# Kernel optimization log

Hardware: AMD Instinct MI355X
Metric: run time of the kernel (lower is better)

## Reference

```python
import jax, jax.numpy as jnp
import numpy as np

EMBED_DIM = 1024
NUM_HEADS = 16
HEAD_DIM = EMBED_DIM // NUM_HEADS


def setup_inputs() -> dict:
    key = jax.random.key(0)
    k1, k2, k3, k4, k5 = jax.random.split(key, 5)
    B, T, C = 4, 2048, EMBED_DIM
    scale = 1.0 / np.sqrt(C)
    return {
        "x": jax.random.normal(k1, (B, T, C), dtype=jnp.float32),
        "W_qkv": jax.random.normal(k2, (3 * C, C), dtype=jnp.float32) * scale,
        "b_qkv": jax.random.normal(k3, (3 * C,), dtype=jnp.float32) * 0.02,
        "W_proj": jax.random.normal(k4, (C, C), dtype=jnp.float32) * scale,
        "b_proj": jax.random.normal(k5, (C,), dtype=jnp.float32) * 0.02,
    }


def reference(x, W_qkv, b_qkv, W_proj, b_proj):
    B, T, C = x.shape
    H, D = NUM_HEADS, HEAD_DIM
    qkv = x @ W_qkv.T + b_qkv                      # [B,T,3C]
    q, k, v = jnp.split(qkv, 3, axis=-1)
    q = q.reshape(B, T, H, D).transpose(0, 2, 1, 3)  # [B,H,T,D]
    k = k.reshape(B, T, H, D).transpose(0, 2, 1, 3)
    v = v.reshape(B, T, H, D).transpose(0, 2, 1, 3)
    scores = jnp.einsum("bhqd,bhkd->bhqk", q, k) / np.sqrt(D)  # [B,H,T,T]
    causal = jnp.tril(jnp.ones((T, T), dtype=bool))
    scores = jnp.where(causal, scores, -jnp.inf)
    attn = jax.nn.softmax(scores, axis=-1)
    out = jnp.einsum("bhqk,bhkd->bhqd", attn, v)   # [B,H,T,D]
    out = out.transpose(0, 2, 1, 3).reshape(B, T, C)
    return out @ W_proj.T + b_proj
```

## Files before the change

kernel.cpp:

```cpp
#include <hip/hip_runtime.h>
#include <math.h>

#define EMBED 1024
#define NHEAD 16
#define HDIM  64
#define SEQT  2048
#define BATCH 4

typedef __bf16 bf16x4 __attribute__((ext_vector_type(4)));
typedef __bf16 bf16x8 __attribute__((ext_vector_type(8)));
typedef float  f32x4  __attribute__((ext_vector_type(4)));

#define AS1 __attribute__((address_space(1)))
#define AS3 __attribute__((address_space(3)))
#define GLD_LDS16(gp, lp) __builtin_amdgcn_global_load_lds( \
    (const AS1 unsigned int*)(gp), (AS3 unsigned int*)(lp), 16, 0, 0)

#define QSCALE 0.180336880f

__device__ __forceinline__ unsigned short f2bf_hw(float f) {
    union { __bf16 h; unsigned short u; } c; c.h = (__bf16)f; return c.u;
}

__global__ __launch_bounds__(256)
void cvt_all(const float* __restrict__ x, const float* __restrict__ wq,
             const float* __restrict__ wp,
             unsigned short* __restrict__ xb, unsigned short* __restrict__ wqb,
             unsigned short* __restrict__ wpb)
{
    const int N1 = 2097152;
    const int N2 = 786432;
    int i = blockIdx.x * 256 + threadIdx.x;
    const float4* src; ushort4* dst; int j;
    if (i < N1)            { src = (const float4*)x;  dst = (ushort4*)xb;  j = i; }
    else if (i < N1 + N2)  { src = (const float4*)wq; dst = (ushort4*)wqb; j = i - N1; }
    else                   { src = (const float4*)wp; dst = (ushort4*)wpb; j = i - N1 - N2; }
    float4 v = src[j];
    ushort4 o;
    o.x = f2bf_hw(v.x); o.y = f2bf_hw(v.y); o.z = f2bf_hw(v.z); o.w = f2bf_hw(v.w);
    dst[j] = o;
}

template<int MODE>
__global__ __launch_bounds__(256)
void gemm_bt_mfma(const unsigned short* __restrict__ A, const unsigned short* __restrict__ Bw,
                  const float* __restrict__ bias,
                  void* out0, void* out1, void* out2,
                  int M, int N, int K)
{
    __shared__ __align__(16) unsigned short Asm[2][128 * 64];
    __shared__ __align__(16) unsigned short Bsm[2][128 * 64];

    const int tid  = threadIdx.x;
    const int lane = tid & 63;
    const int wave = tid >> 6;
    const int wm = wave >> 1, wn = wave & 1;
    const int col = lane & 15, quad = lane >> 4;
    const long m0 = (long)blockIdx.y * 128, n0 = (long)blockIdx.x * 128;

    f32x4 acc[4][4];
#pragma unroll
    for (int mi = 0; mi < 4; mi++)
#pragma unroll
        for (int ni = 0; ni < 4; ni++) acc[mi][ni] = (f32x4){0.f, 0.f, 0.f, 0.f};

    const int srow  = tid >> 3;
    const int gslot = (tid & 7) ^ (srow & 7);
    const unsigned short* Ag = A  + (m0 + srow) * K + gslot * 8;
    const unsigned short* Bg = Bw + (n0 + srow) * K + gslot * 8;

#define STAGE(buf_, kk_) do { \
    _Pragma("unroll") for (int r_ = 0; r_ < 4; r_++) { \
        GLD_LDS16(Ag + (long)(r_ * 32) * K + (kk_), &Asm[buf_][0] + r_ * 2048 + tid * 8); \
        GLD_LDS16(Bg + (long)(r_ * 32) * K + (kk_), &Bsm[buf_][0] + r_ * 2048 + tid * 8); \
    } } while (0)

    const int cs0 = ((quad    ) ^ (col & 7)) * 8;
    const int cs1 = ((quad + 4) ^ (col & 7)) * 8;

    STAGE(0, 0);

    const int iters = K >> 6;
    for (int it = 0; it < iters; it++) {
        const int cur = it & 1;
        __builtin_amdgcn_s_waitcnt(0x0F70);
        __syncthreads();
        if (it + 1 < iters)
            STAGE(cur ^ 1, (it + 1) * 64);

        bf16x8 af[4][2], bf[4][2];
#pragma unroll
        for (int mi = 0; mi < 4; mi++) {
            const int row = wm * 64 + mi * 16 + col;
            af[mi][0] = *(const bf16x8*)&Asm[cur][row * 64 + cs0];
            af[mi][1] = *(const bf16x8*)&Asm[cur][row * 64 + cs1];
        }
#pragma unroll
        for (int ni = 0; ni < 4; ni++) {
            const int row = wn * 64 + ni * 16 + col;
            bf[ni][0] = *(const bf16x8*)&Bsm[cur][row * 64 + cs0];
            bf[ni][1] = *(const bf16x8*)&Bsm[cur][row * 64 + cs1];
        }
#pragma unroll
        for (int mi = 0; mi < 4; mi++)
#pragma unroll
            for (int ni = 0; ni < 4; ni++) {
                acc[mi][ni] = __builtin_amdgcn_mfma_f32_16x16x32_bf16(af[mi][0], bf[ni][0], acc[mi][ni], 0, 0, 0);
                acc[mi][ni] = __builtin_amdgcn_mfma_f32_16x16x32_bf16(af[mi][1], bf[ni][1], acc[mi][ni], 0, 0, 0);
            }
    }
#undef STAGE

#pragma unroll
    for (int mi = 0; mi < 4; mi++) {
#pragma unroll
        for (int ni = 0; ni < 4; ni++) {
            long n = n0 + wn * 64 + ni * 16 + col;
            float bv = bias[n];
#pragma unroll
            for (int r = 0; r < 4; r++) {
                long m = m0 + wm * 64 + mi * 16 + quad * 4 + r;
                float v = acc[mi][ni][r] + bv;
                if (MODE == 0) {
                    ((float*)out0)[m * N + n] = v;
                } else {
                    int which = (int)(n >> 10);
                    int c = (int)(n & 1023);
                    int h = c >> 6, d = c & 63;
                    int b = (int)(m >> 11), t = (int)(m & 2047);
                    long bh = (long)(b * NHEAD + h);
                    if (which == 0)      ((unsigned short*)out0)[(bh * SEQT + t) * HDIM + d] = f2bf_hw(v * QSCALE);
                    else if (which == 1) ((unsigned short*)out1)[(bh * SEQT + t) * HDIM + d] = f2bf_hw(v);
                    else                 ((unsigned short*)out2)[(bh * HDIM + d) * SEQT + t] = f2bf_hw(v);
                }
            }
        }
    }
}

#define PPAD 72

__global__ __launch_bounds__(256, 3)
void flash_attn_mfma4(const unsigned short* __restrict__ Qb,
                      const unsigned short* __restrict__ Kb,
                      const unsigned short* __restrict__ Vt,
                      unsigned short* __restrict__ Ob)
{
    __shared__ __align__(16) unsigned short P_lds[128 * PPAD];
    __shared__ __align__(16) unsigned short K_lds[2][64 * 64];
    __shared__ __align__(16) unsigned short V_lds[2][64 * 64];
    __shared__ __align__(16) float L_lds[128];

    const int tid  = threadIdx.x;
    const int lane = tid & 63;
    const int wave = tid >> 6;
    const int col  = lane & 15;
    const int quad = lane >> 4;

    const int idx = blockIdx.x;
    const int qt = 15 - (idx >> 6);
    const int hb = idx & 63;
    const int h = hb & 15, b = hb >> 4;
    const int q0 = qt * 128;
    const long bh = (long)(b * NHEAD + h);
    const unsigned short* Kbh = Kb + bh * SEQT * HDIM;
    const unsigned short* Vbh = Vt + bh * HDIM * SEQT;
    const int ktiles = 2 * qt + 2;

    const int r0 = tid >> 3,         c0 = (tid & 7) ^ (r0 & 7);
    const int r1 = (tid + 256) >> 3, c1 = (tid & 7) ^ (r1 & 7);

    bf16x8 qf[2][2];
#pragma unroll
    for (int ni = 0; ni < 2; ni++) {
        const unsigned short* qrow = Qb + (bh * SEQT + q0 + wave * 32 + ni * 16 + col) * HDIM;
        qf[ni][0] = *(const bf16x8*)(qrow + quad * 8);
        qf[ni][1] = *(const bf16x8*)(qrow + 32 + quad * 8);
    }

    GLD_LDS16(Kbh + r0 * HDIM + c0 * 8,        &K_lds[0][0] + tid * 8);
    GLD_LDS16(Kbh + r1 * HDIM + c1 * 8,        &K_lds[0][0] + 2048 + tid * 8);
    GLD_LDS16(Vbh + (long)r0 * SEQT + c0 * 8,  &V_lds[0][0] + tid * 8);
    GLD_LDS16(Vbh + (long)r1 * SEQT + c1 * 8,  &V_lds[0][0] + 2048 + tid * 8);

    f32x4 o[2][4];
#pragma unroll
    for (int mi = 0; mi < 2; mi++)
#pragma unroll
        for (int dt = 0; dt < 4; dt++) o[mi][dt] = (f32x4){0.f, 0.f, 0.f, 0.f};
    float rs[2] = {0.f, 0.f};

    const int cswz0 = quad ^ (col & 7);
    const int cswz1 = (quad + 4) ^ (col & 7);

    for (int kt = 0; kt < ktiles; kt++) {
        const int cur = kt & 1;
        __builtin_amdgcn_s_waitcnt(0x0F70);
        __syncthreads();
        if (kt + 1 < ktiles) {
            const int k0n = (kt + 1) * 64, nxt = cur ^ 1;
            GLD_LDS16(Kbh + (k0n + r0) * HDIM + c0 * 8,       &K_lds[nxt][0] + tid * 8);
            GLD_LDS16(Kbh + (k0n + r1) * HDIM + c1 * 8,       &K_lds[nxt][0] + 2048 + tid * 8);
            GLD_LDS16(Vbh + (long)r0 * SEQT + k0n + c0 * 8,   &V_lds[nxt][0] + tid * 8);
            GLD_LDS16(Vbh + (long)r1 * SEQT + k0n + c1 * 8,   &V_lds[nxt][0] + 2048 + tid * 8);
        }

        const unsigned short* Kc = &K_lds[cur][0];
        f32x4 st[4][2];
        __builtin_amdgcn_s_setprio(1);
#pragma unroll
        for (int mt = 0; mt < 4; mt++) {
            const int row = mt * 16 + col;
            bf16x8 kf0 = *(const bf16x8*)&Kc[row * 64 + cswz0 * 8];
            bf16x8 kf1 = *(const bf16x8*)&Kc[row * 64 + cswz1 * 8];
#pragma unroll
            for (int ni = 0; ni < 2; ni++) {
                f32x4 acc = (f32x4){0.f, 0.f, 0.f, 0.f};
                acc = __builtin_amdgcn_mfma_f32_16x16x32_bf16(kf0, qf[ni][0], acc, 0, 0, 0);
                acc = __builtin_amdgcn_mfma_f32_16x16x32_bf16(kf1, qf[ni][1], acc, 0, 0, 0);
                st[mt][ni] = acc;
            }
        }
        __builtin_amdgcn_s_setprio(0);
        const int k0 = kt * 64;
        if (kt >= 2 * qt) {
#pragma unroll
            for (int mt = 0; mt < 4; mt++) {
                const int keybase = k0 + mt * 16 + quad * 4;
#pragma unroll
                for (int ni = 0; ni < 2; ni++) {
                    const int qg = q0 + wave * 32 + ni * 16 + col;
#pragma unroll
                    for (int r = 0; r < 4; r++)
                        if (keybase + r > qg) st[mt][ni][r] = -INFINITY;
                }
            }
        }

#pragma unroll
        for (int mt = 0; mt < 4; mt++)
#pragma unroll
            for (int ni = 0; ni < 2; ni++) {
                f32x4 p;
#pragma unroll
                for (int r = 0; r < 4; r++) p[r] = __builtin_amdgcn_exp2f(st[mt][ni][r]);
                rs[ni] += (p[0] + p[1]) + (p[2] + p[3]);
                bf16x4 pb = __builtin_convertvector(p, bf16x4);
                *(bf16x4*)&P_lds[(wave * 32 + ni * 16 + col) * PPAD + mt * 16 + quad * 4] = pb;
            }

        const unsigned short* Vc = &V_lds[cur][0];
        __builtin_amdgcn_s_setprio(1);
#pragma unroll
        for (int mi = 0; mi < 2; mi++) {
            const unsigned short* prow = &P_lds[(wave * 32 + mi * 16 + col) * PPAD];
            bf16x8 pf0 = *(const bf16x8*)(prow + quad * 8);
            bf16x8 pf1 = *(const bf16x8*)(prow + 32 + quad * 8);
#pragma unroll
            for (int dt = 0; dt < 4; dt++) {
                const int row = dt * 16 + col;
                bf16x8 vf0 = *(const bf16x8*)&Vc[row * 64 + cswz0 * 8];
                bf16x8 vf1 = *(const bf16x8*)&Vc[row * 64 + cswz1 * 8];
                o[mi][dt] = __builtin_amdgcn_mfma_f32_16x16x32_bf16(pf0, vf0, o[mi][dt], 0, 0, 0);
                o[mi][dt] = __builtin_amdgcn_mfma_f32_16x16x32_bf16(pf1, vf1, o[mi][dt], 0, 0, 0);
            }
        }
        __builtin_amdgcn_s_setprio(0);
    }

#pragma unroll
    for (int ni = 0; ni < 2; ni++) {
        rs[ni] += __shfl_xor(rs[ni], 16);
        rs[ni] += __shfl_xor(rs[ni], 32);
        if (quad == 0) L_lds[wave * 32 + ni * 16 + col] = rs[ni];
    }
    __syncthreads();
    f32x4 lf[2];
#pragma unroll
    for (int mi = 0; mi < 2; mi++)
        lf[mi] = *(const f32x4*)&L_lds[wave * 32 + mi * 16 + quad * 4];

#pragma unroll
    for (int mi = 0; mi < 2; mi++)
#pragma unroll
        for (int r = 0; r < 4; r++) {
            float inv = 1.f / lf[mi][r];
            int t = q0 + wave * 32 + mi * 16 + quad * 4 + r;
            unsigned short* orow = Ob + ((long)(b * SEQT + t)) * EMBED + h * HDIM;
#pragma unroll
            for (int dt = 0; dt < 4; dt++)
                orow[dt * 16 + col] = f2bf_hw(o[mi][dt][r] * inv);
        }
}

extern "C" void kernel_launch(void* const* d_in, const int* in_sizes, int n_in,
                              void* d_out, int out_size, void* d_ws, size_t ws_size,
                              hipStream_t stream)
{
    const float* x     = (const float*)d_in[0];
    const float* Wqkv  = (const float*)d_in[1];
    const float* bqkv  = (const float*)d_in[2];
    const float* Wproj = (const float*)d_in[3];
    const float* bproj = (const float*)d_in[4];
    float* out = (float*)d_out;

    const long Mbt = (long)BATCH * SEQT;
    const long per = (long)BATCH * NHEAD * SEQT * HDIM;

    unsigned short* xb  = (unsigned short*)d_ws;
    unsigned short* wqb = xb  + per;
    unsigned short* wpb = wqb + 3 * EMBED * EMBED;
    unsigned short* Qb  = wpb + EMBED * EMBED;
    unsigned short* Kb  = Qb + per;
    unsigned short* Vt  = Kb + per;
    unsigned short* Ob  = Vt + per;

    cvt_all<<<12288, 256, 0, stream>>>(x, Wqkv, Wproj, xb, wqb, wpb);

    dim3 g1(3 * EMBED / 128, Mbt / 128);
    gemm_bt_mfma<1><<<g1, 256, 0, stream>>>(xb, wqb, bqkv, Qb, Kb, Vt,
                                            (int)Mbt, 3 * EMBED, EMBED);

    flash_attn_mfma4<<<1024, 256, 0, stream>>>(Qb, Kb, Vt, Ob);

    dim3 g3(EMBED / 128, Mbt / 128);
    gemm_bt_mfma<0><<<g3, 256, 0, stream>>>(Ob, wpb, bproj, out, nullptr, nullptr,
                                            (int)Mbt, EMBED, EMBED);
}
```

Before: 250.7 us.

## Register-prefetch single-buffered K/V tiles and interleave causal block order

New measurement: 395.8 us. 1.58x slower.

```diff
diff --git a/kernel.cpp b/kernel.cpp
--- a/kernel.cpp
+++ b/kernel.cpp
@@ -10,6 +10,7 @@
 typedef __bf16 bf16x4 __attribute__((ext_vector_type(4)));
 typedef __bf16 bf16x8 __attribute__((ext_vector_type(8)));
 typedef float  f32x4  __attribute__((ext_vector_type(4)));
+typedef unsigned short u16x8 __attribute__((ext_vector_type(8)));
 
 #define AS1 __attribute__((address_space(1)))
 #define AS3 __attribute__((address_space(3)))
@@ -140,15 +141,15 @@
 
 #define PPAD 72
 
-__global__ __launch_bounds__(256, 3)
-void flash_attn_mfma4(const unsigned short* __restrict__ Qb,
+__global__ __launch_bounds__(256, 4)
+void flash_attn_mfma5(const unsigned short* __restrict__ Qb,
                       const unsigned short* __restrict__ Kb,
                       const unsigned short* __restrict__ Vt,
                       unsigned short* __restrict__ Ob)
 {
     __shared__ __align__(16) unsigned short P_lds[128 * PPAD];
-    __shared__ __align__(16) unsigned short K_lds[2][64 * 64];
-    __shared__ __align__(16) unsigned short V_lds[2][64 * 64];
+    __shared__ __align__(16) unsigned short K_lds[64 * 64];
+    __shared__ __align__(16) unsigned short V_lds[64 * 64];
     __shared__ __align__(16) float L_lds[128];
 
     const int tid  = threadIdx.x;
@@ -158,7 +159,8 @@
     const int quad = lane >> 4;
 
     const int idx = blockIdx.x;
-    const int qt = 15 - (idx >> 6);
+    const int g = idx >> 6;
+    const int qt = (g & 1) ? (g >> 1) : (15 - (g >> 1));
     const int hb = idx & 63;
     const int h = hb & 15, b = hb >> 4;
     const int q0 = qt * 128;
@@ -167,8 +169,17 @@
     const unsigned short* Vbh = Vt + bh * HDIM * SEQT;
     const int ktiles = 2 * qt + 2;
 
-    const int r0 = tid >> 3,         c0 = (tid & 7) ^ (r0 & 7);
-    const int r1 = (tid + 256) >> 3, c1 = (tid & 7) ^ (r1 & 7);
+    const int r0   = tid >> 3;
+    const int slot = tid & 7;
+    const int ws   = (slot ^ (r0 & 7)) * 8;
+    unsigned short* kw0 = &K_lds[r0 * 64 + ws];
+    unsigned short* kw1 = &K_lds[(r0 + 32) * 64 + ws];
+    unsigned short* vw0 = &V_lds[r0 * 64 + ws];
+    unsigned short* vw1 = &V_lds[(r0 + 32) * 64 + ws];
+    const unsigned short* Kg0 = Kbh + r0 * HDIM + slot * 8;
+    const unsigned short* Kg1 = Kbh + (r0 + 32) * HDIM + slot * 8;
+    const unsigned short* Vg0 = Vbh + (long)r0 * SEQT + slot * 8;
+    const unsigned short* Vg1 = Vbh + (long)(r0 + 32) * SEQT + slot * 8;
 
     bf16x8 qf[2][2];
 #pragma unroll
@@ -178,10 +189,15 @@
         qf[ni][1] = *(const bf16x8*)(qrow + 32 + quad * 8);
     }
 
-    GLD_LDS16(Kbh + r0 * HDIM + c0 * 8,        &K_lds[0][0] + tid * 8);
-    GLD_LDS16(Kbh + r1 * HDIM + c1 * 8,        &K_lds[0][0] + 2048 + tid * 8);
-    GLD_LDS16(Vbh + (long)r0 * SEQT + c0 * 8,  &V_lds[0][0] + tid * 8);
-    GLD_LDS16(Vbh + (long)r1 * SEQT + c1 * 8,  &V_lds[0][0] + 2048 + tid * 8);
+    {
+        u16x8 kr0 = *(const u16x8*)Kg0;
+        u16x8 kr1 = *(const u16x8*)Kg1;
+        u16x8 vr0 = *(const u16x8*)Vg0;
+        u16x8 vr1 = *(const u16x8*)Vg1;
+        *(u16x8*)kw0 = kr0; *(u16x8*)kw1 = kr1;
+        *(u16x8*)vw0 = vr0; *(u16x8*)vw1 = vr1;
+    }
+    __syncthreads();
 
     f32x4 o[2][4];
 #pragma unroll
@@ -193,26 +209,24 @@
     const int cswz0 = quad ^ (col & 7);
     const int cswz1 = (quad + 4) ^ (col & 7);
 
+    u16x8 kr0, kr1, vr0, vr1;
     for (int kt = 0; kt < ktiles; kt++) {
-        const int cur = kt & 1;
-        __builtin_amdgcn_s_waitcnt(0x0F70);
-        __syncthreads();
         if (kt + 1 < ktiles) {
-            const int k0n = (kt + 1) * 64, nxt = cur ^ 1;
-            GLD_LDS16(Kbh + (k0n + r0) * HDIM + c0 * 8,       &K_lds[nxt][0] + tid * 8);
-            GLD_LDS16(Kbh + (k0n + r1) * HDIM + c1 * 8,       &K_lds[nxt][0] + 2048 + tid * 8);
-            GLD_LDS16(Vbh + (long)r0 * SEQT + k0n + c0 * 8,   &V_lds[nxt][0] + tid * 8);
-            GLD_LDS16(Vbh + (long)r1 * SEQT + k0n + c1 * 8,   &V_lds[nxt][0] + 2048 + tid * 8);
-        }
-
-        const unsigned short* Kc = &K_lds[cur][0];
+            const int t1 = (kt + 1) * 64;
+            kr0 = *(const u16x8*)(Kg0 + (long)t1 * HDIM);
+            kr1 = *(const u16x8*)(Kg1 + (long)t1 * HDIM);
+            vr0 = *(const u16x8*)(Vg0 + t1);
+            vr1 = *(const u16x8*)(Vg1 + t1);
+        }
+        __builtin_amdgcn_sched_barrier(0);
+
         f32x4 st[4][2];
         __builtin_amdgcn_s_setprio(1);
 #pragma unroll
         for (int mt = 0; mt < 4; mt++) {
             const int row = mt * 16 + col;
-            bf16x8 kf0 = *(const bf16x8*)&Kc[row * 64 + cswz0 * 8];
-            bf16x8 kf1 = *(const bf16x8*)&Kc[row * 64 + cswz1 * 8];
+            bf16x8 kf0 = *(const bf16x8*)&K_lds[row * 64 + cswz0 * 8];
+            bf16x8 kf1 = *(const bf16x8*)&K_lds[row * 64 + cswz1 * 8];
 #pragma unroll
             for (int ni = 0; ni < 2; ni++) {
                 f32x4 acc = (f32x4){0.f, 0.f, 0.f, 0.f};
@@ -249,7 +263,6 @@
                 *(bf16x4*)&P_lds[(wave * 32 + ni * 16 + col) * PPAD + mt * 16 + quad * 4] = pb;
             }
 
-        const unsigned short* Vc = &V_lds[cur][0];
         __builtin_amdgcn_s_setprio(1);
 #pragma unroll
         for (int mi = 0; mi < 2; mi++) {
@@ -259,13 +272,20 @@
 #pragma unroll
             for (int dt = 0; dt < 4; dt++) {
                 const int row = dt * 16 + col;
-                bf16x8 vf0 = *(const bf16x8*)&Vc[row * 64 + cswz0 * 8];
-                bf16x8 vf1 = *(const bf16x8*)&Vc[row * 64 + cswz1 * 8];
+                bf16x8 vf0 = *(const bf16x8*)&V_lds[row * 64 + cswz0 * 8];
+                bf16x8 vf1 = *(const bf16x8*)&V_lds[row * 64 + cswz1 * 8];
                 o[mi][dt] = __builtin_amdgcn_mfma_f32_16x16x32_bf16(pf0, vf0, o[mi][dt], 0, 0, 0);
                 o[mi][dt] = __builtin_amdgcn_mfma_f32_16x16x32_bf16(pf1, vf1, o[mi][dt], 0, 0, 0);
             }
         }
         __builtin_amdgcn_s_setprio(0);
+
+        __syncthreads();
+        if (kt + 1 < ktiles) {
+            *(u16x8*)kw0 = kr0; *(u16x8*)kw1 = kr1;
+            *(u16x8*)vw0 = vr0; *(u16x8*)vw1 = vr1;
+        }
+        __syncthreads();
     }
 
 #pragma unroll
@@ -321,7 +341,7 @@
     gemm_bt_mfma<1><<<g1, 256, 0, stream>>>(xb, wqb, bqkv, Qb, Kb, Vt,
                                             (int)Mbt, 3 * EMBED, EMBED);
 
-    flash_attn_mfma4<<<1024, 256, 0, stream>>>(Qb, Kb, Vt, Ob);
+    flash_attn_mfma5<<<1024, 256, 0, stream>>>(Qb, Kb, Vt, Ob);
 
     dim3 g3(EMBED / 128, Mbt / 128);
     gemm_bt_mfma<0><<<g3, 256, 0, stream>>>(Ob, wpb, bproj, out, nullptr, nullptr,
```

## Switch flash attention to 32x32x16 MFMA and keep P in registers

Applied to the files above, without the earlier changes.

After: 256.9 us. 1.02x slower.

```diff
diff --git a/kernel.cpp b/kernel.cpp
--- a/kernel.cpp
+++ b/kernel.cpp
@@ -10,6 +10,7 @@
 typedef __bf16 bf16x4 __attribute__((ext_vector_type(4)));
 typedef __bf16 bf16x8 __attribute__((ext_vector_type(8)));
 typedef float  f32x4  __attribute__((ext_vector_type(4)));
+typedef float  f32x16 __attribute__((ext_vector_type(16)));
 
 #define AS1 __attribute__((address_space(1)))
 #define AS3 __attribute__((address_space(3)))
@@ -20,6 +21,9 @@
 
 __device__ __forceinline__ unsigned short f2bf_hw(float f) {
     union { __bf16 h; unsigned short u; } c; c.h = (__bf16)f; return c.u;
+}
+__device__ __forceinline__ unsigned pk2(float a, float b) {
+    union { __bf16 h[2]; unsigned u; } c; c.h[0] = (__bf16)a; c.h[1] = (__bf16)b; return c.u;
 }
 
 __global__ __launch_bounds__(256)
@@ -138,24 +142,21 @@
     }
 }
 
-#define PPAD 72
-
 __global__ __launch_bounds__(256, 3)
-void flash_attn_mfma4(const unsigned short* __restrict__ Qb,
+void flash_attn_mfma6(const unsigned short* __restrict__ Qb,
                       const unsigned short* __restrict__ Kb,
                       const unsigned short* __restrict__ Vt,
                       unsigned short* __restrict__ Ob)
 {
-    __shared__ __align__(16) unsigned short P_lds[128 * PPAD];
     __shared__ __align__(16) unsigned short K_lds[2][64 * 64];
     __shared__ __align__(16) unsigned short V_lds[2][64 * 64];
-    __shared__ __align__(16) float L_lds[128];
 
     const int tid  = threadIdx.x;
     const int lane = tid & 63;
     const int wave = tid >> 6;
-    const int col  = lane & 15;
-    const int quad = lane >> 4;
+    const int lq   = lane & 31;
+    const int hi   = lane >> 5;
+    const int l7   = lane & 7;
 
     const int idx = blockIdx.x;
     const int qt = 15 - (idx >> 6);
@@ -166,32 +167,26 @@
     const unsigned short* Kbh = Kb + bh * SEQT * HDIM;
     const unsigned short* Vbh = Vt + bh * HDIM * SEQT;
     const int ktiles = 2 * qt + 2;
-
-    const int r0 = tid >> 3,         c0 = (tid & 7) ^ (r0 & 7);
-    const int r1 = (tid + 256) >> 3, c1 = (tid & 7) ^ (r1 & 7);
-
-    bf16x8 qf[2][2];
-#pragma unroll
-    for (int ni = 0; ni < 2; ni++) {
-        const unsigned short* qrow = Qb + (bh * SEQT + q0 + wave * 32 + ni * 16 + col) * HDIM;
-        qf[ni][0] = *(const bf16x8*)(qrow + quad * 8);
-        qf[ni][1] = *(const bf16x8*)(qrow + 32 + quad * 8);
-    }
-
-    GLD_LDS16(Kbh + r0 * HDIM + c0 * 8,        &K_lds[0][0] + tid * 8);
-    GLD_LDS16(Kbh + r1 * HDIM + c1 * 8,        &K_lds[0][0] + 2048 + tid * 8);
-    GLD_LDS16(Vbh + (long)r0 * SEQT + c0 * 8,  &V_lds[0][0] + tid * 8);
-    GLD_LDS16(Vbh + (long)r1 * SEQT + c1 * 8,  &V_lds[0][0] + 2048 + tid * 8);
-
-    f32x4 o[2][4];
-#pragma unroll
-    for (int mi = 0; mi < 2; mi++)
-#pragma unroll
-        for (int dt = 0; dt < 4; dt++) o[mi][dt] = (f32x4){0.f, 0.f, 0.f, 0.f};
-    float rs[2] = {0.f, 0.f};
-
-    const int cswz0 = quad ^ (col & 7);
-    const int cswz1 = (quad + 4) ^ (col & 7);
+    const int qg = q0 + wave * 32 + lq;
+
+    const int r0 = tid >> 3;
+    const int cs = (tid & 7) ^ (r0 & 7);
+
+    bf16x8 qf[4];
+    {
+        const unsigned short* qrow = Qb + (bh * SEQT + qg) * HDIM;
+#pragma unroll
+        for (int c = 0; c < 4; c++)
+            qf[c] = *(const bf16x8*)(qrow + c * 16 + hi * 8);
+    }
+
+    GLD_LDS16(Kbh + r0 * HDIM + cs * 8,              &K_lds[0][0] + tid * 8);
+    GLD_LDS16(Kbh + (r0 + 32) * HDIM + cs * 8,       &K_lds[0][0] + 2048 + tid * 8);
+    GLD_LDS16(Vbh + (long)r0 * SEQT + cs * 8,        &V_lds[0][0] + tid * 8);
+    GLD_LDS16(Vbh + (long)(r0 + 32) * SEQT + cs * 8, &V_lds[0][0] + 2048 + tid * 8);
+
+    f32x16 ot0 = {}, ot1 = {};
+    float rs = 0.f;
 
     for (int kt = 0; kt < ktiles; kt++) {
         const int cur = kt & 1;
@@ -199,98 +194,92 @@
         __syncthreads();
         if (kt + 1 < ktiles) {
             const int k0n = (kt + 1) * 64, nxt = cur ^ 1;
-            GLD_LDS16(Kbh + (k0n + r0) * HDIM + c0 * 8,       &K_lds[nxt][0] + tid * 8);
-            GLD_LDS16(Kbh + (k0n + r1) * HDIM + c1 * 8,       &K_lds[nxt][0] + 2048 + tid * 8);
-            GLD_LDS16(Vbh + (long)r0 * SEQT + k0n + c0 * 8,   &V_lds[nxt][0] + tid * 8);
-            GLD_LDS16(Vbh + (long)r1 * SEQT + k0n + c1 * 8,   &V_lds[nxt][0] + 2048 + tid * 8);
+            GLD_LDS16(Kbh + (k0n + r0) * HDIM + cs * 8,            &K_lds[nxt][0] + tid * 8);
+            GLD_LDS16(Kbh + (k0n + r0 + 32) * HDIM + cs * 8,       &K_lds[nxt][0] + 2048 + tid * 8);
+            GLD_LDS16(Vbh + (long)r0 * SEQT + k0n + cs * 8,        &V_lds[nxt][0] + tid * 8);
+            GLD_LDS16(Vbh + (long)(r0 + 32) * SEQT + k0n + cs * 8, &V_lds[nxt][0] + 2048 + tid * 8);
         }
 
         const unsigned short* Kc = &K_lds[cur][0];
-        f32x4 st[4][2];
+        const unsigned short* Vc = &V_lds[cur][0];
+
+        f32x16 st0 = {}, st1 = {};
         __builtin_amdgcn_s_setprio(1);
 #pragma unroll
-        for (int mt = 0; mt < 4; mt++) {
-            const int row = mt * 16 + col;
-            bf16x8 kf0 = *(const bf16x8*)&Kc[row * 64 + cswz0 * 8];
-            bf16x8 kf1 = *(const bf16x8*)&Kc[row * 64 + cswz1 * 8];
-#pragma unroll
-            for (int ni = 0; ni < 2; ni++) {
-                f32x4 acc = (f32x4){0.f, 0.f, 0.f, 0.f};
-                acc = __builtin_amdgcn_mfma_f32_16x16x32_bf16(kf0, qf[ni][0], acc, 0, 0, 0);
-                acc = __builtin_amdgcn_mfma_f32_16x16x32_bf16(kf1, qf[ni][1], acc, 0, 0, 0);
-                st[mt][ni] = acc;
+        for (int c = 0; c < 4; c++) {
+            const int sl = ((2 * c + hi) ^ l7) * 8;
+            bf16x8 ka = *(const bf16x8*)&Kc[lq * 64 + sl];
+            bf16x8 kb = *(const bf16x8*)&Kc[(lq + 32) * 64 + sl];
+            st0 = __builtin_amdgcn_mfma_f32_32x32x16_bf16(ka, qf[c], st0, 0, 0, 0);
+            st1 = __builtin_amdgcn_mfma_f32_32x32x16_bf16(kb, qf[c], st1, 0, 0, 0);
+        }
+        __builtin_amdgcn_s_setprio(0);
+
+        if (kt >= 2 * qt) {
+            const int kbase = kt * 64;
+#pragma unroll
+            for (int r = 0; r < 16; r++) {
+                const int rowl = (r & 3) + 8 * (r >> 2) + 4 * hi;
+                if (kbase + rowl > qg)      st0[r] = -INFINITY;
+                if (kbase + 32 + rowl > qg) st1[r] = -INFINITY;
             }
         }
-        __builtin_amdgcn_s_setprio(0);
-        const int k0 = kt * 64;
-        if (kt >= 2 * qt) {
-#pragma unroll
-            for (int mt = 0; mt < 4; mt++) {
-                const int keybase = k0 + mt * 16 + quad * 4;
-#pragma unroll
-                for (int ni = 0; ni < 2; ni++) {
-                    const int qg = q0 + wave * 32 + ni * 16 + col;
-#pragma unroll
-                    for (int r = 0; r < 4; r++)
-                        if (keybase + r > qg) st[mt][ni][r] = -INFINITY;
-                }
-            }
-        }
-
-#pragma unroll
-        for (int mt = 0; mt < 4; mt++)
-#pragma unroll
-            for (int ni = 0; ni < 2; ni++) {
-                f32x4 p;
-#pragma unroll
-                for (int r = 0; r < 4; r++) p[r] = __builtin_amdgcn_exp2f(st[mt][ni][r]);
-                rs[ni] += (p[0] + p[1]) + (p[2] + p[3]);
-                bf16x4 pb = __builtin_convertvector(p, bf16x4);
-                *(bf16x4*)&P_lds[(wave * 32 + ni * 16 + col) * PPAD + mt * 16 + quad * 4] = pb;
-            }
-
-        const unsigned short* Vc = &V_lds[cur][0];
-        __builtin_amdgcn_s_setprio(1);
-#pragma unroll
-        for (int mi = 0; mi < 2; mi++) {
-            const unsigned short* prow = &P_lds[(wave * 32 + mi * 16 + col) * PPAD];
-            bf16x8 pf0 = *(const bf16x8*)(prow + quad * 8);
-            bf16x8 pf1 = *(const bf16x8*)(prow + 32 + quad * 8);
-#pragma unroll
-            for (int dt = 0; dt < 4; dt++) {
-                const int row = dt * 16 + col;
-                bf16x8 vf0 = *(const bf16x8*)&Vc[row * 64 + cswz0 * 8];
-                bf16x8 vf1 = *(const bf16x8*)&Vc[row * 64 + cswz1 * 8];
-                o[mi][dt] = __builtin_amdgcn_mfma_f32_16x16x32_bf16(pf0, vf0, o[mi][dt], 0, 0, 0);
-                o[mi][dt] = __builtin_amdgcn_mfma_f32_16x16x32_bf16(pf1, vf1, o[mi][dt], 0, 0, 0);
-            }
-        }
-        __builtin_amdgcn_s_setprio(0);
-    }
-
-#pragma unroll
-    for (int ni = 0; ni < 2; ni++) {
-        rs[ni] += __shfl_xor(rs[ni], 16);
-        rs[ni] += __shfl_xor(rs[ni], 32);
-        if (quad == 0) L_lds[wave * 32 + ni * 16 + col] = rs[ni];
-    }
-    __syncthreads();
-    f32x4 lf[2];
-#pragma unroll
-    for (int mi = 0; mi < 2; mi++)
-        lf[mi] = *(const f32x4*)&L_lds[wave * 32 + mi * 16 + quad * 4];
-
-#pragma unroll
-    for (int mi = 0; mi < 2; mi++)
-#pragma unroll
-        for (int r = 0; r < 4; r++) {
-            float inv = 1.f / lf[mi][r];
-            int t = q0 + wave * 32 + mi * 16 + quad * 4 + r;
-            unsigned short* orow = Ob + ((long)(b * SEQT + t)) * EMBED + h * HDIM;
-#pragma unroll
-            for (int dt = 0; dt < 4; dt++)
-                orow[dt * 16 + col] = f2bf_hw(o[mi][dt][r] * inv);
-        }
+
+#pragma unroll
+        for (int r = 0; r < 16; r++) {
+            st0[r] = __builtin_amdgcn_exp2f(st0[r]);
+            st1[r] = __builtin_amdgcn_exp2f(st1[r]);
+            rs += st0[r] + st1[r];
+        }
+
+#pragma unroll
+        for (int c = 0; c < 4; c++) {
+            const f32x16 ps = (c < 2) ? st0 : st1;
+            const int cc = (c & 1) * 8;
+            unsigned W00 = pk2(ps[cc + 0], ps[cc + 1]);
+            unsigned W01 = pk2(ps[cc + 2], ps[cc + 3]);
+            unsigned W10 = pk2(ps[cc + 4], ps[cc + 5]);
+            unsigned W11 = pk2(ps[cc + 6], ps[cc + 7]);
+            unsigned s0 = hi ? W00 : W10;
+            unsigned s1 = hi ? W01 : W11;
+            unsigned x0 = (unsigned)__shfl_xor((int)s0, 32);
+            unsigned x1 = (unsigned)__shfl_xor((int)s1, 32);
+            union { unsigned u[4]; bf16x8 v; } pb;
+            pb.u[0] = hi ? x0  : W00;
+            pb.u[1] = hi ? x1  : W01;
+            pb.u[2] = hi ? W10 : x0;
+            pb.u[3] = hi ? W11 : x1;
+            const int sl = ((2 * c + hi) ^ l7) * 8;
+            bf16x8 va = *(const bf16x8*)&Vc[lq * 64 + sl];
+            bf16x8 vb = *(const bf16x8*)&Vc[(lq + 32) * 64 + sl];
+            __builtin_amdgcn_s_setprio(1);
+            ot0 = __builtin_amdgcn_mfma_f32_32x32x16_bf16(va, pb.v, ot0, 0, 0, 0);
+            ot1 = __builtin_amdgcn_mfma_f32_32x32x16_bf16(vb, pb.v, ot1, 0, 0, 0);
+            __builtin_amdgcn_s_setprio(0);
+        }
+    }
+
+    rs += __shfl_xor(rs, 32);
+    const float inv = 1.f / rs;
+
+    unsigned short* orow = Ob + ((long)(b * SEQT + qg)) * EMBED + h * HDIM;
+#pragma unroll
+    for (int g = 0; g < 4; g++) {
+        {
+            const int d0 = 8 * g + 4 * hi;
+            bf16x4 w;
+#pragma unroll
+            for (int e = 0; e < 4; e++) w[e] = (__bf16)(ot0[4 * g + e] * inv);
+            *(bf16x4*)(orow + d0) = w;
+        }
+        {
+            const int d0 = 32 + 8 * g + 4 * hi;
+            bf16x4 w;
+#pragma unroll
+            for (int e = 0; e < 4; e++) w[e] = (__bf16)(ot1[4 * g + e] * inv);
+            *(bf16x4*)(orow + d0) = w;
+        }
+    }
 }
 
 extern "C" void kernel_launch(void* const* d_in, const int* in_sizes, int n_in,
@@ -321,7 +310,7 @@
     gemm_bt_mfma<1><<<g1, 256, 0, stream>>>(xb, wqb, bqkv, Qb, Kb, Vt,
                                             (int)Mbt, 3 * EMBED, EMBED);
 
-    flash_attn_mfma4<<<1024, 256, 0, stream>>>(Qb, Kb, Vt, Ob);
+    flash_attn_mfma6<<<1024, 256, 0, stream>>>(Qb, Kb, Vt, Ob);
 
     dim3 g3(EMBED / 128, Mbt / 128);
     gemm_bt_mfma<0><<<g3, 256, 0, stream>>>(Ob, wpb, bproj, out, nullptr, nullptr,
```
